# Performance work log

Hardware: AMD Instinct MI355X
Metric: run time of the kernel (lower is better)

The kernel has to match this reference:

```python
import math
import jax, jax.numpy as jnp
import numpy as np

B, N, C, H = 4, 1025, 768, 12
D = C // H                      # head_dim = 64
SCALE = D ** -0.5
NUM = N // 4                    # CSA block size = 256
FUSE_T = math.ceil(0.1 * (N - 1))     # 103
ENH_T = math.ceil(0.1 * (N - 1))      # 103


def _csa_mask():
    # has_cls=True: tokens 1..4*NUM get block id 0..3; cls (idx 0) gets -1 (unmasked).
    bid = (jnp.arange(N) - 1) // NUM
    same = (bid[:, None] == bid[None, :]) & (bid[:, None] >= 0) & (bid[:, None] < 4)
    return jnp.where(same, -jnp.inf, 0.0).astype(jnp.float32)  # [N, N]


def setup_inputs() -> dict:
    key = jax.random.key(0)
    kx, kq, kw, kb = jax.random.split(key, 4)
    x = jax.random.normal(kx, (B, N, C), dtype=jnp.float32)
    w_qkv = jax.random.normal(kq, (3 * C, C), dtype=jnp.float32) * 0.02  # Linear(C, 3C, bias=False)
    w_out = jax.random.normal(kw, (C, C), dtype=jnp.float32) * 0.02
    b_out = jax.random.normal(kb, (C,), dtype=jnp.float32) * 0.02
    return {"x": x, "w_qkv": w_qkv, "w_out": w_out, "b_out": b_out}


def reference(x, w_qkv, w_out, b_out):
    b, n, c = x.shape
    h, d = H, c // H
    # qkv projection + rearrange 'b n (qkv h d) -> qkv b h n d'
    qkv = (x @ w_qkv.T).reshape(b, n, 3, h, d).transpose(2, 0, 3, 1, 4)
    q, k, v = qkv[0], qkv[1], qkv[2]          # each [b, h, n, d]

    scores = jnp.einsum('bhxd,bhyd->bhxy', q, k) * SCALE + _csa_mask()
    att = jax.nn.softmax(scores, axis=-1)     # [b, h, n, n]  (dropout=0, eval)

    ctx = jnp.einsum('bhxy,bhyd->bhxd', att, v)
    out = ctx.transpose(0, 2, 1, 3).reshape(b, n, c) @ w_out.T + b_out

    # cls-attention-driven token selection
    cls_attn = att[:, :, 0, 1:].mean(axis=1)  # [b, n-1]
    _, fuse_idx = jax.lax.top_k(-cls_attn, FUSE_T)   # smallest, ascending
    _, enh_idx = jax.lax.top_k(cls_attn, ENH_T)      # largest, descending
    fuse_index = jnp.broadcast_to(fuse_idx[:, :, None], (b, FUSE_T, c))
    enhance_index = jnp.broadcast_to(enh_idx[:, :, None], (b, ENH_T, c))
    return (out, enhance_index, enh_idx, fuse_index, fuse_idx, cls_attn)
```

## Files before the change

kernel.cpp:

```cpp
#include <hip/hip_runtime.h>


#define B_  4
#define N_  1025
#define C_  768
#define H_  12
#define D_  64
#define M_TOT (B_ * N_)
#define M_PAD 4224
#define KEXP 2304
#define NPAD 1088

#define OFF_EIND 3148800
#define OFF_EIDX 3465216
#define OFF_FIND 3465628
#define OFF_FIDX 3782044
#define OFF_CLS  3782456

#define WS_F64   0
#define WS_XS    196608
#define WS_QKVB  5062656
#define WS_OUTB  7716864
#define WS_QE    8601600
#define WS_KE    11943936
#define WS_VT    15286272

#define DQ0 0
#define DMS 3072
#define DLG 39936
#define DMX 89136
#define DZ  89184
#define DMV 89232

#define SPLIT_A_ITEMS (M_PAD * 192)
#define SPLIT_B1_ITEMS (2304 * 192)
#define SPLIT_B2_ITEMS (768 * 192)
#define SPLIT_TOTAL (SPLIT_A_ITEMS + SPLIT_B1_ITEMS + SPLIT_B2_ITEMS)
#define SPLIT_BLOCKS ((SPLIT_TOTAL + 255) / 256)

#define QKV_BLOCKS 594
#define OUT_BLOCKS 198

typedef short s16x8 __attribute__((ext_vector_type(8)));
typedef float f32x4 __attribute__((ext_vector_type(4)));

__device__ inline unsigned short f2bf(float f) {
    unsigned u = __float_as_uint(f);
    u += 0x7FFF + ((u >> 16) & 1);
    return (unsigned short)(u >> 16);
}
__device__ inline float bf2f(unsigned short h) {
    return __uint_as_float(((unsigned)h) << 16);
}

__device__ __forceinline__ void gl2lds16(const unsigned short* g, unsigned short* l) {
    __builtin_amdgcn_global_load_lds(
        (const __attribute__((address_space(1))) unsigned int*)g,
        (__attribute__((address_space(3))) unsigned int*)l,
        16, 0, 0);
}

__device__ inline void gemm_decode(int lid, int NT, int& m, int& n) {
    int gi = lid / (8 * NT);
    int r  = lid % (8 * NT);
    int base = gi * 8;
    int gsize = (33 - base < 8) ? (33 - base) : 8;
    n = r / gsize;
    m = base + r % gsize;
}

__global__ __launch_bounds__(256) void fused_split_q0_kernel(
    const float* __restrict__ x, const float* __restrict__ w_qkv,
    const float* __restrict__ w_out,
    unsigned short* __restrict__ xs, unsigned short* __restrict__ qkvB,
    unsigned short* __restrict__ outB, double* __restrict__ dws)
{
    if (blockIdx.x >= SPLIT_BLOCKS) {
        const int t = threadIdx.x;
        const int wg = (blockIdx.x - SPLIT_BLOCKS) * 4 + (t >> 6);
        const int lane = t & 63;
        const int b = wg / 768, rem = wg - b * 768;
        const float* x0 = x + (size_t)b * N_ * C_;
        const float* wr = w_qkv + (size_t)rem * C_;
        double s = 0.0;
        #pragma unroll
        for (int i = 0; i < 12; i++) {
            int c = lane + i*64;
            s += (double)x0[c] * (double)wr[c];
        }
        #pragma unroll
        for (int o = 1; o < 64; o <<= 1) s += __shfl_xor(s, o);
        if (lane == 0) dws[DQ0 + wg] = s * 0.125;
        return;
    }
    int idx = blockIdx.x * 256 + threadIdx.x;
    if (idx < SPLIT_A_ITEMS) {
        int m = idx / 192, c4 = (idx - m * 192) * 4;
        ushort4 hi = make_ushort4(0,0,0,0), lo = hi;
        if (m < M_TOT) {
            float4 f = *(const float4*)&x[(size_t)m * C_ + c4];
            hi.x = f2bf(f.x); hi.y = f2bf(f.y); hi.z = f2bf(f.z); hi.w = f2bf(f.w);
            lo.x = f2bf(f.x - bf2f(hi.x)); lo.y = f2bf(f.y - bf2f(hi.y));
            lo.z = f2bf(f.z - bf2f(hi.z)); lo.w = f2bf(f.w - bf2f(hi.w));
        }
        unsigned short* d = xs + (size_t)m * KEXP + c4;
        *(ushort4*)(d)        = hi;
        *(ushort4*)(d + 768)  = hi;
        *(ushort4*)(d + 1536) = lo;
        return;
    }
    idx -= SPLIT_A_ITEMS;
    const float* src;
    unsigned short* dst;
    if (idx < SPLIT_B1_ITEMS) { src = w_qkv; dst = qkvB; }
    else { idx -= SPLIT_B1_ITEMS; if (idx >= SPLIT_B2_ITEMS) return; src = w_out; dst = outB; }
    int m = idx / 192, c4 = (idx - m * 192) * 4;
    float4 f = *(const float4*)&src[(size_t)m * C_ + c4];
    ushort4 hi, lo;
    hi.x = f2bf(f.x); hi.y = f2bf(f.y); hi.z = f2bf(f.z); hi.w = f2bf(f.w);
    lo.x = f2bf(f.x - bf2f(hi.x)); lo.y = f2bf(f.y - bf2f(hi.y));
    lo.z = f2bf(f.z - bf2f(hi.z)); lo.w = f2bf(f.w - bf2f(hi.w));
    unsigned short* d = dst + (size_t)m * KEXP + c4;
    *(ushort4*)(d)        = hi;
    *(ushort4*)(d + 768)  = lo;
    *(ushort4*)(d + 1536) = hi;
}

__global__ __launch_bounds__(256) void fused_gemm_qkv_ms_kernel(
    const unsigned short* __restrict__ A, const unsigned short* __restrict__ Bm,
    unsigned short* __restrict__ qe, unsigned short* __restrict__ ke,
    unsigned short* __restrict__ vtp,
    const float* __restrict__ w_qkv, double* __restrict__ dws)
{
    __shared__ unsigned short AsF[3*4096];
    __shared__ unsigned short BsF[3*4096];

    if (blockIdx.x >= QKV_BLOCKS) {
        double* q0s = (double*)AsF;
        const int lid = blockIdx.x - QKV_BLOCKS;
        const int cb = lid % 3;
        const int h  = (lid / 3) % 12;
        const int b  = lid / 36;
        const int t = threadIdx.x;
        const int c = cb * 256 + t;
        if (t < 64) q0s[t] = dws[DQ0 + (b*H_ + h)*64 + t];
        __syncthreads();
        const float* wk = w_qkv + (size_t)(C_ + h*64) * C_ + c;
        double s = 0.0;
        #pragma unroll 8
        for (int d = 0; d < 64; d++) s += q0s[d] * (double)wk[(size_t)d * C_];
        dws[DMS + ((size_t)(b*H_ + h))*768 + c] = s;
        return;
    }

    int mi, ni;
    gemm_decode(blockIdx.x, 18, mi, ni);
    const int n0 = ni * 128;
    const int m0 = mi * 128;
    const int t = threadIdx.x;
    const int lane = t & 63, wv = t >> 6;
    const int wr = wv >> 1, wc = wv & 1;
    const int q4 = lane >> 4, r = lane & 15;
    const int lrr = lane >> 2;
    const int lcc = ((lane & 3) ^ ((lane >> 3) & 3)) * 8;
    const int sw  = (q4 ^ ((r >> 1) & 3)) * 8;

    f32x4 acc[4][4];
    #pragma unroll
    for (int i = 0; i < 4; i++)
        #pragma unroll
        for (int j = 0; j < 4; j++)
            #pragma unroll
            for (int e = 0; e < 4; e++) acc[i][j][e] = 0.f;

    const unsigned short* gA = A  + (size_t)(m0 + wv*16 + lrr) * KEXP + lcc;
    const unsigned short* gB = Bm + (size_t)(n0 + wv*16 + lrr) * KEXP + lcc;

    auto STAGE = [&](int kt, int o) {
        const unsigned short* a = gA + kt * 32;
        const unsigned short* b = gB + kt * 32;
        gl2lds16(a,                       AsF + o + wv*512);
        gl2lds16(a + (size_t)64 * KEXP,   AsF + o + 2048 + wv*512);
        gl2lds16(b,                       BsF + o + wv*512);
        gl2lds16(b + (size_t)64 * KEXP,   BsF + o + 2048 + wv*512);
    };

    STAGE(0, 0);
    STAGE(1, 4096);

    int cb = 0;
    for (int it = 0; it < 72; ++it) {
        if (it + 1 < 72) asm volatile("s_waitcnt vmcnt(4)" ::: "memory");
        else             asm volatile("s_waitcnt vmcnt(0)" ::: "memory");
        __builtin_amdgcn_s_barrier();
        asm volatile("" ::: "memory");
        __builtin_amdgcn_sched_barrier(0);
        if (it + 2 < 72) {
            int nb = (cb >= 1) ? cb - 1 : cb + 2;
            STAGE(it + 2, nb * 4096);
        }
        const int cbuf = cb * 4096;
        s16x8 af[4], bfr[4];
        #pragma unroll
        for (int i = 0; i < 4; i++) {
            af[i]  = *(const s16x8*)&AsF[cbuf + (wr*64 + i*16 + r)*32 + sw];
            bfr[i] = *(const s16x8*)&BsF[cbuf + (wc*64 + i*16 + r)*32 + sw];
        }
        #pragma unroll
        for (int i = 0; i < 4; i++)
            #pragma unroll
            for (int j = 0; j < 4; j++)
                acc[i][j] = __builtin_amdgcn_mfma_f32_16x16x32_bf16(af[i], bfr[j], acc[i][j], 0, 0, 0);
        cb = (cb < 2) ? cb + 1 : 0;
    }

    const int sel = n0 / C_;
    const int off = n0 % C_;
    const float scl = (sel == 0) ? 0.125f : 1.0f;
    #pragma unroll
    for (int i = 0; i < 4; i++) {
        #pragma unroll
        for (int rr = 0; rr < 4; rr++) {
            int gm = m0 + wr*64 + i*16 + q4*4 + rr;
            if (gm < M_TOT) {
                int bb = gm / N_, n = gm - bb * N_;
                #pragma unroll
                for (int j = 0; j < 4; j++) {
                    int col = off + wc*64 + j*16 + r;
                    int h = col >> 6, d = col & 63;
                    float val = acc[i][j][rr] * scl;
                    unsigned short hi = f2bf(val);
                    unsigned short lo = f2bf(val - bf2f(hi));
                    size_t bh = (size_t)(bb*H_ + h);
                    if (sel <= 1) {
                        unsigned short* dst = (sel == 0 ? qe : ke) + (bh*NPAD + n)*128;
                        dst[d]      = hi;
                        dst[64 + d] = lo;
                    } else {
                        unsigned short* dst = vtp + bh*128*NPAD;
                        dst[(size_t)d*NPAD + n]        = hi;
                        dst[(size_t)(64 + d)*NPAD + n] = lo;
                    }
                }
            }
        }
    }
}

__global__ __launch_bounds__(256, 4) void fused_attn_logits_kernel(
    const unsigned short* __restrict__ qe, const unsigned short* __restrict__ ke,
    const unsigned short* __restrict__ vtp, unsigned short* __restrict__ ctxs,
    const float* __restrict__ x, double* __restrict__ dws)
{
    __shared__ unsigned short KP[64*128];
    __shared__ unsigned short VP[128*64];

    if (blockIdx.x >= 816) {
        double* xsd = (double*)KP;
        const int lid = blockIdx.x - 816;
        const int j = lid % 1025, b = lid / 1025;
        const int t = threadIdx.x;
        const int w = t >> 6, lane = t & 63;
        const float* xr = x + ((size_t)b * N_ + j) * C_;
        for (int c = t; c < C_; c += 256) xsd[c] = (double)xr[c];
        __syncthreads();
        for (int hh = 0; hh < 3; hh++) {
            int h = w + hh * 4;
            const double* ms = dws + DMS + ((size_t)(b*H_ + h))*768;
            double s = 0.0;
            #pragma unroll
            for (int i = 0; i < 12; i++) {
                int c = lane + i*64;
                s += xsd[c] * ms[c];
            }
            #pragma unroll
            for (int o = 1; o < 64; o <<= 1) s += __shfl_xor(s, o);
            if (lane == 0) dws[DLG + ((size_t)(b*H_ + h))*1025 + j] = s;
        }
        return;
    }

    const int qt = blockIdx.x / 48;
    const int g  = blockIdx.x - qt * 48;
    const int h = g % 12, b = g / 12;
    const int t = threadIdx.x;
    const int w = t >> 6, lane = t & 63;
    const int quad = lane >> 4, r16 = lane & 15;
    const size_t bh = (size_t)(b*H_ + h);

    s16x8 ah0, ah1, al0, al1;
    {
        const unsigned short* qrow = qe + (bh*NPAD + qt*64 + w*16 + r16) * 128;
        const int q8 = quad * 8;
        ah0 = *(const s16x8*)(qrow + q8);
        ah1 = *(const s16x8*)(qrow + 32 + q8);
        al0 = *(const s16x8*)(qrow + 64 + q8);
        al1 = *(const s16x8*)(qrow + 96 + q8);
    }

    int qu;
    {
        int rlo = qt*64, rhi = min(qt*64 + 63, N_ - 1);
        if (rlo == 0) qu = -2;
        else { int b1 = (rlo-1)>>8, b2 = (rhi-1)>>8; qu = (b1==b2) ? b1 : -2; }
    }

    float m_run[4], l_run[4];
    f32x4 ctx[4];
    #pragma unroll
    for (int i = 0; i < 4; i++) {
        m_run[i] = -1e30f; l_run[i] = 0.f;
        #pragma unroll
        for (int e = 0; e < 4; e++) ctx[i][e] = 0.f;
    }

    const unsigned short* keb = ke  + (bh*NPAD) * 128;
    const unsigned short* vtb = vtp + bh*(size_t)128*NPAD;

    const int kchunk = (t & 15) ^ ((t >> 4) & 15);
    const int vchunk = (t & 7)  ^ ((t >> 3) & 7);
    const unsigned short* kg0 = keb + (size_t)(t >> 4) * 128 + kchunk * 8;
    const unsigned short* vg0 = vtb + (size_t)(t >> 3) * NPAD + vchunk * 8;

    const int s0 = (quad ^ r16) << 3;
    const int sv = (quad ^ (r16 & 7)) << 3;
    unsigned short* Pew = KP + w*16*128;

    for (int kt = 0; kt < 17; kt++) {
        if (qu >= 0 && kt > 0) {
            int clo = kt*64, chi = min(kt*64 + 63, N_ - 1);
            int b1 = (clo-1)>>8, b2 = (chi-1)>>8;
            if (b1 == b2 && b1 == qu) continue;
        }

        __syncthreads();
        {
            const unsigned short* kg = kg0 + (size_t)kt * 64 * 128;
            const unsigned short* vg = vg0 + kt * 64;
            #pragma unroll
            for (int i = 0; i < 4; i++) {
                gl2lds16(kg + i * 2048,              KP + i*2048 + w*512);
                gl2lds16(vg + (size_t)i * 32 * NPAD, VP + i*2048 + w*512);
            }
        }
        __syncthreads();

        f32x4 st[4];
        #pragma unroll
        for (int j = 0; j < 4; j++)
            #pragma unroll
            for (int e = 0; e < 4; e++) st[j][e] = 0.f;
        __builtin_amdgcn_s_setprio(1);
        #pragma unroll
        for (int j = 0; j < 4; j++) {
            const unsigned short* kr = &KP[(j*16 + r16) * 128];
            s16x8 bh0 = *(const s16x8*)&kr[s0];
            s16x8 bh1 = *(const s16x8*)&kr[s0 ^ 32];
            s16x8 bl0 = *(const s16x8*)&kr[s0 ^ 64];
            s16x8 bl1 = *(const s16x8*)&kr[s0 ^ 96];
            st[j] = __builtin_amdgcn_mfma_f32_16x16x32_bf16(ah0, bh0, st[j], 0,0,0);
            st[j] = __builtin_amdgcn_mfma_f32_16x16x32_bf16(ah1, bh1, st[j], 0,0,0);
            st[j] = __builtin_amdgcn_mfma_f32_16x16x32_bf16(ah0, bl0, st[j], 0,0,0);
            st[j] = __builtin_amdgcn_mfma_f32_16x16x32_bf16(ah1, bl1, st[j], 0,0,0);
            st[j] = __builtin_amdgcn_mfma_f32_16x16x32_bf16(al0, bh0, st[j], 0,0,0);
            st[j] = __builtin_amdgcn_mfma_f32_16x16x32_bf16(al1, bh1, st[j], 0,0,0);
        }
        __builtin_amdgcn_s_setprio(0);

        float pv[4][4];
        float alpha[4];
        #pragma unroll
        for (int reg = 0; reg < 4; reg++) {
            int gr = qt*64 + w*16 + quad*4 + reg;
            int qb = (gr >= 1) ? ((gr - 1) >> 8) : -1;
            float mx = -1e30f;
            float vv[4];
            #pragma unroll
            for (int j = 0; j < 4; j++) {
                int gc = kt*64 + j*16 + r16;
                bool ok = (gr < N_) && (gc < N_) &&
                          !((gr >= 1) && (gc >= 1) && (((gc - 1) >> 8) == qb));
                vv[j] = ok ? st[j][reg] : -1e30f;
                mx = fmaxf(mx, vv[j]);
            }
            mx = fmaxf(mx, __shfl_xor(mx, 1));
            mx = fmaxf(mx, __shfl_xor(mx, 2));
            mx = fmaxf(mx, __shfl_xor(mx, 4));
            mx = fmaxf(mx, __shfl_xor(mx, 8));
            float mnew = fmaxf(m_run[reg], mx);
            alpha[reg] = __expf(m_run[reg] - mnew);
            m_run[reg] = mnew;
            float ps = 0.f;
            #pragma unroll
            for (int j = 0; j < 4; j++) {
                float pp = (vv[j] > -1e29f) ? __expf(vv[j] - mnew) : 0.f;
                pv[reg][j] = pp; ps += pp;
            }
            ps += __shfl_xor(ps, 1);
            ps += __shfl_xor(ps, 2);
            ps += __shfl_xor(ps, 4);
            ps += __shfl_xor(ps, 8);
            l_run[reg] = l_run[reg] * alpha[reg] + ps;
        }

        __syncthreads();

        #pragma unroll
        for (int reg = 0; reg < 4; reg++) {
            int lrow = quad*4 + reg;
            #pragma unroll
            for (int j = 0; j < 4; j++) {
                float pp = pv[reg][j];
                unsigned short ph = f2bf(pp);
                unsigned short pl = f2bf(pp - bf2f(ph));
                int colh = j*16 + r16;
                int coll = 64 + colh;
                Pew[lrow*128 + (((colh >> 3) ^ lrow) << 3) + (colh & 7)] = ph;
                Pew[lrow*128 + (((coll >> 3) ^ lrow) << 3) + (coll & 7)] = pl;
            }
        }

        #pragma unroll
        for (int nj = 0; nj < 4; nj++)
            #pragma unroll
            for (int reg = 0; reg < 4; reg++)
                ctx[nj][reg] *= alpha[reg];

        {
            const unsigned short* pr = &Pew[r16 * 128];
            s16x8 ph0 = *(const s16x8*)&pr[s0];
            s16x8 ph1 = *(const s16x8*)&pr[s0 ^ 32];
            s16x8 pl0 = *(const s16x8*)&pr[s0 ^ 64];
            s16x8 pl1 = *(const s16x8*)&pr[s0 ^ 96];
            __builtin_amdgcn_s_setprio(1);
            #pragma unroll
            for (int nj = 0; nj < 4; nj++) {
                const unsigned short* vh = &VP[(nj*16 + r16) * 64];
                const unsigned short* vl = &VP[(64 + nj*16 + r16) * 64];
                s16x8 vh0 = *(const s16x8*)&vh[sv];
                s16x8 vh1 = *(const s16x8*)&vh[sv ^ 32];
                s16x8 vl0 = *(const s16x8*)&vl[sv];
                s16x8 vl1 = *(const s16x8*)&vl[sv ^ 32];
                ctx[nj] = __builtin_amdgcn_mfma_f32_16x16x32_bf16(ph0, vh0, ctx[nj], 0,0,0);
                ctx[nj] = __builtin_amdgcn_mfma_f32_16x16x32_bf16(ph1, vh1, ctx[nj], 0,0,0);
                ctx[nj] = __builtin_amdgcn_mfma_f32_16x16x32_bf16(ph0, vl0, ctx[nj], 0,0,0);
                ctx[nj] = __builtin_amdgcn_mfma_f32_16x16x32_bf16(ph1, vl1, ctx[nj], 0,0,0);
                ctx[nj] = __builtin_amdgcn_mfma_f32_16x16x32_bf16(pl0, vh0, ctx[nj], 0,0,0);
                ctx[nj] = __builtin_amdgcn_mfma_f32_16x16x32_bf16(pl1, vh1, ctx[nj], 0,0,0);
            }
            __builtin_amdgcn_s_setprio(0);
        }
    }

    #pragma unroll
    for (int reg = 0; reg < 4; reg++) {
        int gr = qt*64 + w*16 + quad*4 + reg;
        if (gr < N_) {
            float inv = 1.0f / l_run[reg];
            size_t row = (size_t)(b*N_ + gr) * KEXP;
            #pragma unroll
            for (int nj = 0; nj < 4; nj++) {
                float val = ctx[nj][reg] * inv;
                unsigned short hi = f2bf(val);
                unsigned short lo = f2bf(val - bf2f(hi));
                int c = h*64 + nj*16 + r16;
                ctxs[row + c]        = hi;
                ctxs[row + 768 + c]  = hi;
                ctxs[row + 1536 + c] = lo;
            }
        }
    }
}

__global__ __launch_bounds__(256) void fused_gemm_out_reduce_kernel(
    const unsigned short* __restrict__ A, const unsigned short* __restrict__ Bm,
    const float* __restrict__ bias, float* __restrict__ out,
    double* __restrict__ dws)
{
    __shared__ unsigned short AsF[3*4096];
    __shared__ unsigned short BsF[3*4096];

    if (blockIdx.x >= OUT_BLOCKS) {
        double* red = (double*)AsF;
        const int lid = blockIdx.x - OUT_BLOCKS;
        const int h = lid % 12, b = lid / 12;
        const int t = threadIdx.x;
        const double* lg = dws + DLG + ((size_t)(b*H_ + h))*1025;
        double mloc = -1e300;
        for (int j = t; j < N_; j += 256) mloc = fmax(mloc, lg[j]);
        red[t] = mloc; __syncthreads();
        for (int o = 128; o > 0; o >>= 1) {
            if (t < o) red[t] = fmax(red[t], red[t+o]);
            __syncthreads();
        }
        double mx = red[0]; __syncthreads();
        double sloc = 0.0;
        for (int j = t; j < N_; j += 256) sloc += exp(lg[j] - mx);
        red[t] = sloc; __syncthreads();
        for (int o = 128; o > 0; o >>= 1) {
            if (t < o) red[t] += red[t+o];
            __syncthreads();
        }
        if (t == 0) {
            dws[DMX + b*H_ + h] = mx;
            dws[DZ  + b*H_ + h] = red[0];
        }
        return;
    }

    int mi, ni;
    gemm_decode(blockIdx.x, 6, mi, ni);
    const int n0 = ni * 128;
    const int m0 = mi * 128;
    const int t = threadIdx.x;
    const int lane = t & 63, wv = t >> 6;
    const int wr = wv >> 1, wc = wv & 1;
    const int q4 = lane >> 4, r = lane & 15;
    const int lrr = lane >> 2;
    const int lcc = ((lane & 3) ^ ((lane >> 3) & 3)) * 8;
    const int sw  = (q4 ^ ((r >> 1) & 3)) * 8;

    f32x4 acc[4][4];
    #pragma unroll
    for (int i = 0; i < 4; i++)
        #pragma unroll
        for (int j = 0; j < 4; j++)
            #pragma unroll
            for (int e = 0; e < 4; e++) acc[i][j][e] = 0.f;

    const unsigned short* gA = A  + (size_t)(m0 + wv*16 + lrr) * KEXP + lcc;
    const unsigned short* gB = Bm + (size_t)(n0 + wv*16 + lrr) * KEXP + lcc;

    auto STAGE = [&](int kt, int o) {
        const unsigned short* a = gA + kt * 32;
        const unsigned short* b = gB + kt * 32;
        gl2lds16(a,                       AsF + o + wv*512);
        gl2lds16(a + (size_t)64 * KEXP,   AsF + o + 2048 + wv*512);
        gl2lds16(b,                       BsF + o + wv*512);
        gl2lds16(b + (size_t)64 * KEXP,   BsF + o + 2048 + wv*512);
    };

    STAGE(0, 0);
    STAGE(1, 4096);

    int cb = 0;
    for (int it = 0; it < 72; ++it) {
        if (it + 1 < 72) asm volatile("s_waitcnt vmcnt(4)" ::: "memory");
        else             asm volatile("s_waitcnt vmcnt(0)" ::: "memory");
        __builtin_amdgcn_s_barrier();
        asm volatile("" ::: "memory");
        __builtin_amdgcn_sched_barrier(0);
        if (it + 2 < 72) {
            int nb = (cb >= 1) ? cb - 1 : cb + 2;
            STAGE(it + 2, nb * 4096);
        }
        const int cbuf = cb * 4096;
        s16x8 af[4], bfr[4];
        #pragma unroll
        for (int i = 0; i < 4; i++) {
            af[i]  = *(const s16x8*)&AsF[cbuf + (wr*64 + i*16 + r)*32 + sw];
            bfr[i] = *(const s16x8*)&BsF[cbuf + (wc*64 + i*16 + r)*32 + sw];
        }
        #pragma unroll
        for (int i = 0; i < 4; i++)
            #pragma unroll
            for (int j = 0; j < 4; j++)
                acc[i][j] = __builtin_amdgcn_mfma_f32_16x16x32_bf16(af[i], bfr[j], acc[i][j], 0, 0, 0);
        cb = (cb < 2) ? cb + 1 : 0;
    }

    #pragma unroll
    for (int i = 0; i < 4; i++) {
        #pragma unroll
        for (int rr = 0; rr < 4; rr++) {
            int gm = m0 + wr*64 + i*16 + q4*4 + rr;
            if (gm < M_TOT) {
                #pragma unroll
                for (int j = 0; j < 4; j++) {
                    int col = n0 + wc*64 + j*16 + r;
                    out[(size_t)gm * C_ + col] = acc[i][j][rr] + bias[col];
                }
            }
        }
    }
}

__global__ __launch_bounds__(256) void cls_score_kernel(
    const double* __restrict__ dwsr, double* __restrict__ dws,
    float* __restrict__ out)
{
    const int idx = blockIdx.x * 256 + threadIdx.x;
    const int b = idx >> 10, t = idx & 1023;
    double s = 0.0;
    #pragma unroll
    for (int h = 0; h < H_; h++) {
        double mx = dwsr[DMX + b*H_ + h];
        double Z  = dwsr[DZ  + b*H_ + h];
        double lg = dwsr[DLG + ((size_t)(b*H_ + h))*1025 + (t + 1)];
        s += exp(lg - mx) / Z;
    }
    s *= (1.0 / 12.0);
    dws[DMV + idx] = s;
    out[OFF_CLS + (size_t)b*1024 + t] = (float)s;
}

__global__ __launch_bounds__(256) void cls_rank_kernel(
    const double* __restrict__ dws, float* __restrict__ out)
{
    __shared__ double mv[1024];
    const int q = blockIdx.x, b = blockIdx.y;
    const int tid = threadIdx.x;
    for (int i = tid; i < 1024; i += 256) mv[i] = dws[DMV + b*1024 + i];
    __syncthreads();
    const int t = q*256 + tid;
    const double v = mv[t];
    int cd = 0, ca = 0;
    #pragma unroll 8
    for (int j = 0; j < 1024; j++) {
        double u = mv[j];
        bool tie = (u == v) && (j < t);
        cd += (u > v) || tie;
        ca += (u < v) || tie;
    }
    if (cd < 103) out[OFF_EIDX + (size_t)b*103 + cd] = (float)t;
    if (ca < 103) out[OFF_FIDX + (size_t)b*103 + ca] = (float)t;
}

__global__ __launch_bounds__(256) void cls_fill_kernel(float* __restrict__ out)
{
    const int PER = 103 * 192;
    int idx = blockIdx.x * 256 + threadIdx.x;
    if (idx >= 2 * 4 * PER) return;
    int sel = idx / (4 * PER);
    int r   = idx - sel * 4 * PER;
    int b   = r / PER;
    int rem = r - b * PER;
    int e   = rem / 192;
    int c4  = (rem - e * 192) * 4;
    float val = out[(sel ? OFF_FIDX : OFF_EIDX) + (size_t)b*103 + e];
    float* dst = out + (sel ? OFF_FIND : OFF_EIND) + ((size_t)b*103 + e)*768 + c4;
    *(float4*)dst = make_float4(val, val, val, val);
}

extern "C" void kernel_launch(void* const* d_in, const int* in_sizes, int n_in,
                              void* d_out, int out_size, void* d_ws, size_t ws_size,
                              hipStream_t stream)
{
    const float* x     = (const float*)d_in[0];
    const float* w_qkv = (const float*)d_in[1];
    const float* w_out = (const float*)d_in[2];
    const float* b_out = (const float*)d_in[3];
    float* out = (float*)d_out;
    float* ws  = (float*)d_ws;

    double* dws = (double*)(ws + WS_F64);
    unsigned short* xs   = (unsigned short*)(ws + WS_XS);
    unsigned short* qkvB = (unsigned short*)(ws + WS_QKVB);
    unsigned short* outB = (unsigned short*)(ws + WS_OUTB);
    unsigned short* qe   = (unsigned short*)(ws + WS_QE);
    unsigned short* ke   = (unsigned short*)(ws + WS_KE);
    unsigned short* vtp  = (unsigned short*)(ws + WS_VT);

    fused_split_q0_kernel<<<SPLIT_BLOCKS + 768, 256, 0, stream>>>(
        x, w_qkv, w_out, xs, qkvB, outB, dws);

    fused_gemm_qkv_ms_kernel<<<QKV_BLOCKS + 144, 256, 0, stream>>>(
        xs, qkvB, qe, ke, vtp, w_qkv, dws);

    fused_attn_logits_kernel<<<816 + 4100, 256, 0, stream>>>(
        qe, ke, vtp, xs, x, dws);

    fused_gemm_out_reduce_kernel<<<OUT_BLOCKS + 48, 256, 0, stream>>>(
        xs, outB, b_out, out, dws);

    cls_score_kernel<<<16, 256, 0, stream>>>(dws, dws, out);
    cls_rank_kernel<<<dim3(4, B_), 256, 0, stream>>>(dws, out);
    cls_fill_kernel<<<618, 256, 0, stream>>>(out);
}
```

Before: 345.8 us.

## Halve out-GEMM M tile and fuse cls score, rank, and fill tails

The output projection GEMM moves from 128x128 to 64x128 tiles, giving 396 blocks instead of 198 so more of the CUs have work. Each wave now owns a 64x32 output slice, and the kernel uses smaller A buffers and a launch-bounds occupancy hint. The three small cls kernels (score, rank, index fill) become one kernel, which removes two launches and the intermediate buffer of mean scores. In exchange, each of the 4 rank blocks per batch recomputes all 1024 scores, and the selected threads write their 768-wide index rows serially.

```diff
diff --git a/kernel.cpp b/kernel.cpp
--- a/kernel.cpp
+++ b/kernel.cpp
@@ -30,7 +30,6 @@
 #define DLG 39936
 #define DMX 89136
 #define DZ  89184
-#define DMV 89232
 
 #define SPLIT_A_ITEMS (M_PAD * 192)
 #define SPLIT_B1_ITEMS (2304 * 192)
@@ -39,7 +38,9 @@
 #define SPLIT_BLOCKS ((SPLIT_TOTAL + 255) / 256)
 
 #define QKV_BLOCKS 594
-#define OUT_BLOCKS 198
+#define OUT_MT 66
+#define OUT_NT 6
+#define OUT_BLOCKS (OUT_MT * OUT_NT)
 
 typedef short s16x8 __attribute__((ext_vector_type(8)));
 typedef float f32x4 __attribute__((ext_vector_type(4)));
@@ -65,6 +66,15 @@
     int r  = lid % (8 * NT);
     int base = gi * 8;
     int gsize = (33 - base < 8) ? (33 - base) : 8;
+    n = r / gsize;
+    m = base + r % gsize;
+}
+
+__device__ inline void gemm_decode2(int lid, int MT, int NT, int& m, int& n) {
+    int gi = lid / (8 * NT);
+    int r  = lid % (8 * NT);
+    int base = gi * 8;
+    int gsize = (MT - base < 8) ? (MT - base) : 8;
     n = r / gsize;
     m = base + r % gsize;
 }
@@ -472,12 +482,12 @@
     }
 }
 
-__global__ __launch_bounds__(256) void fused_gemm_out_reduce_kernel(
+__global__ __launch_bounds__(256, 4) void fused_gemm_out_reduce_kernel(
     const unsigned short* __restrict__ A, const unsigned short* __restrict__ Bm,
     const float* __restrict__ bias, float* __restrict__ out,
     double* __restrict__ dws)
 {
-    __shared__ unsigned short AsF[3*4096];
+    __shared__ unsigned short AsF[3*2048];
     __shared__ unsigned short BsF[3*4096];
 
     if (blockIdx.x >= OUT_BLOCKS) {
@@ -509,62 +519,61 @@
     }
 
     int mi, ni;
-    gemm_decode(blockIdx.x, 6, mi, ni);
+    gemm_decode2(blockIdx.x, OUT_MT, OUT_NT, mi, ni);
     const int n0 = ni * 128;
-    const int m0 = mi * 128;
+    const int m0 = mi * 64;
     const int t = threadIdx.x;
     const int lane = t & 63, wv = t >> 6;
-    const int wr = wv >> 1, wc = wv & 1;
     const int q4 = lane >> 4, r = lane & 15;
     const int lrr = lane >> 2;
     const int lcc = ((lane & 3) ^ ((lane >> 3) & 3)) * 8;
     const int sw  = (q4 ^ ((r >> 1) & 3)) * 8;
 
-    f32x4 acc[4][4];
+    f32x4 acc[4][2];
     #pragma unroll
     for (int i = 0; i < 4; i++)
         #pragma unroll
-        for (int j = 0; j < 4; j++)
+        for (int j = 0; j < 2; j++)
             #pragma unroll
             for (int e = 0; e < 4; e++) acc[i][j][e] = 0.f;
 
     const unsigned short* gA = A  + (size_t)(m0 + wv*16 + lrr) * KEXP + lcc;
     const unsigned short* gB = Bm + (size_t)(n0 + wv*16 + lrr) * KEXP + lcc;
 
-    auto STAGE = [&](int kt, int o) {
+    auto STAGE = [&](int kt, int buf) {
         const unsigned short* a = gA + kt * 32;
         const unsigned short* b = gB + kt * 32;
-        gl2lds16(a,                       AsF + o + wv*512);
-        gl2lds16(a + (size_t)64 * KEXP,   AsF + o + 2048 + wv*512);
-        gl2lds16(b,                       BsF + o + wv*512);
-        gl2lds16(b + (size_t)64 * KEXP,   BsF + o + 2048 + wv*512);
+        gl2lds16(a,                       AsF + buf*2048 + wv*512);
+        gl2lds16(b,                       BsF + buf*4096 + wv*512);
+        gl2lds16(b + (size_t)64 * KEXP,   BsF + buf*4096 + 2048 + wv*512);
     };
 
     STAGE(0, 0);
-    STAGE(1, 4096);
+    STAGE(1, 1);
 
     int cb = 0;
     for (int it = 0; it < 72; ++it) {
-        if (it + 1 < 72) asm volatile("s_waitcnt vmcnt(4)" ::: "memory");
+        if (it + 1 < 72) asm volatile("s_waitcnt vmcnt(3)" ::: "memory");
         else             asm volatile("s_waitcnt vmcnt(0)" ::: "memory");
         __builtin_amdgcn_s_barrier();
         asm volatile("" ::: "memory");
         __builtin_amdgcn_sched_barrier(0);
         if (it + 2 < 72) {
             int nb = (cb >= 1) ? cb - 1 : cb + 2;
-            STAGE(it + 2, nb * 4096);
-        }
-        const int cbuf = cb * 4096;
-        s16x8 af[4], bfr[4];
-        #pragma unroll
-        for (int i = 0; i < 4; i++) {
-            af[i]  = *(const s16x8*)&AsF[cbuf + (wr*64 + i*16 + r)*32 + sw];
-            bfr[i] = *(const s16x8*)&BsF[cbuf + (wc*64 + i*16 + r)*32 + sw];
-        }
+            STAGE(it + 2, nb);
+        }
+        const int cA = cb * 2048, cB = cb * 4096;
+        s16x8 af[4], bfr[2];
         #pragma unroll
         for (int i = 0; i < 4; i++)
-            #pragma unroll
-            for (int j = 0; j < 4; j++)
+            af[i]  = *(const s16x8*)&AsF[cA + (i*16 + r)*32 + sw];
+        #pragma unroll
+        for (int j = 0; j < 2; j++)
+            bfr[j] = *(const s16x8*)&BsF[cB + (wv*32 + j*16 + r)*32 + sw];
+        #pragma unroll
+        for (int i = 0; i < 4; i++)
+            #pragma unroll
+            for (int j = 0; j < 2; j++)
                 acc[i][j] = __builtin_amdgcn_mfma_f32_16x16x32_bf16(af[i], bfr[j], acc[i][j], 0, 0, 0);
         cb = (cb < 2) ? cb + 1 : 0;
     }
@@ -573,11 +582,11 @@
     for (int i = 0; i < 4; i++) {
         #pragma unroll
         for (int rr = 0; rr < 4; rr++) {
-            int gm = m0 + wr*64 + i*16 + q4*4 + rr;
+            int gm = m0 + i*16 + q4*4 + rr;
             if (gm < M_TOT) {
                 #pragma unroll
-                for (int j = 0; j < 4; j++) {
-                    int col = n0 + wc*64 + j*16 + r;
+                for (int j = 0; j < 2; j++) {
+                    int col = n0 + wv*32 + j*16 + r;
                     out[(size_t)gm * C_ + col] = acc[i][j][rr] + bias[col];
                 }
             }
@@ -585,35 +594,30 @@
     }
 }
 
-__global__ __launch_bounds__(256) void cls_score_kernel(
-    const double* __restrict__ dwsr, double* __restrict__ dws,
-    float* __restrict__ out)
-{
-    const int idx = blockIdx.x * 256 + threadIdx.x;
-    const int b = idx >> 10, t = idx & 1023;
-    double s = 0.0;
-    #pragma unroll
-    for (int h = 0; h < H_; h++) {
-        double mx = dwsr[DMX + b*H_ + h];
-        double Z  = dwsr[DZ  + b*H_ + h];
-        double lg = dwsr[DLG + ((size_t)(b*H_ + h))*1025 + (t + 1)];
-        s += exp(lg - mx) / Z;
-    }
-    s *= (1.0 / 12.0);
-    dws[DMV + idx] = s;
-    out[OFF_CLS + (size_t)b*1024 + t] = (float)s;
-}
-
-__global__ __launch_bounds__(256) void cls_rank_kernel(
+__global__ __launch_bounds__(256) void cls_tail_kernel(
     const double* __restrict__ dws, float* __restrict__ out)
 {
     __shared__ double mv[1024];
     const int q = blockIdx.x, b = blockIdx.y;
     const int tid = threadIdx.x;
-    for (int i = tid; i < 1024; i += 256) mv[i] = dws[DMV + b*1024 + i];
+
+    for (int i = tid; i < 1024; i += 256) {
+        double s = 0.0;
+        #pragma unroll
+        for (int h = 0; h < H_; h++) {
+            double mx = dws[DMX + b*H_ + h];
+            double Z  = dws[DZ  + b*H_ + h];
+            double lg = dws[DLG + ((size_t)(b*H_ + h))*1025 + (i + 1)];
+            s += exp(lg - mx) / Z;
+        }
+        mv[i] = s * (1.0 / 12.0);
+    }
     __syncthreads();
+
     const int t = q*256 + tid;
     const double v = mv[t];
+    out[OFF_CLS + (size_t)b*1024 + t] = (float)v;
+
     int cd = 0, ca = 0;
     #pragma unroll 8
     for (int j = 0; j < 1024; j++) {
@@ -622,24 +626,19 @@
         cd += (u > v) || tie;
         ca += (u < v) || tie;
     }
-    if (cd < 103) out[OFF_EIDX + (size_t)b*103 + cd] = (float)t;
-    if (ca < 103) out[OFF_FIDX + (size_t)b*103 + ca] = (float)t;
-}
-
-__global__ __launch_bounds__(256) void cls_fill_kernel(float* __restrict__ out)
-{
-    const int PER = 103 * 192;
-    int idx = blockIdx.x * 256 + threadIdx.x;
-    if (idx >= 2 * 4 * PER) return;
-    int sel = idx / (4 * PER);
-    int r   = idx - sel * 4 * PER;
-    int b   = r / PER;
-    int rem = r - b * PER;
-    int e   = rem / 192;
-    int c4  = (rem - e * 192) * 4;
-    float val = out[(sel ? OFF_FIDX : OFF_EIDX) + (size_t)b*103 + e];
-    float* dst = out + (sel ? OFF_FIND : OFF_EIND) + ((size_t)b*103 + e)*768 + c4;
-    *(float4*)dst = make_float4(val, val, val, val);
+    const float tv = (float)t;
+    if (cd < 103) {
+        out[OFF_EIDX + (size_t)b*103 + cd] = tv;
+        float* dst = out + OFF_EIND + ((size_t)b*103 + cd)*768;
+        float4 v4 = make_float4(tv, tv, tv, tv);
+        for (int c4 = 0; c4 < 768; c4 += 4) *(float4*)(dst + c4) = v4;
+    }
+    if (ca < 103) {
+        out[OFF_FIDX + (size_t)b*103 + ca] = tv;
+        float* dst = out + OFF_FIND + ((size_t)b*103 + ca)*768;
+        float4 v4 = make_float4(tv, tv, tv, tv);
+        for (int c4 = 0; c4 < 768; c4 += 4) *(float4*)(dst + c4) = v4;
+    }
 }
 
 extern "C" void kernel_launch(void* const* d_in, const int* in_sizes, int n_in,
@@ -673,7 +672,5 @@
     fused_gemm_out_reduce_kernel<<<OUT_BLOCKS + 48, 256, 0, stream>>>(
         xs, outB, b_out, out, dws);
 
-    cls_score_kernel<<<16, 256, 0, stream>>>(dws, dws, out);
-    cls_rank_kernel<<<dim3(4, B_), 256, 0, stream>>>(dws, out);
-    cls_fill_kernel<<<618, 256, 0, stream>>>(out);
-}
+    cls_tail_kernel<<<dim3(4, B_), 256, 0, stream>>>(dws, out);
+}
```

Result: slower. 362.8 us (+4.9%).
